# Kernel tuning notes

Measured on AMD Instinct MI355X. Metric: run time of the kernel, lower is better.

The kernel has to match this reference:

```python
import jax, jax.numpy as jnp
import numpy as np

DIM = 256   # state dimension
T = 8192    # number of time steps
B = 32      # batch of initial conditions
DT = 0.01   # time-grid spacing


def make_A(dim):
    # Faithful to MagnusLadder.__init__: diag=-0.1, superdiag=+0.5, subdiag=-0.5
    A = np.zeros((dim, dim), dtype=np.float32)
    np.fill_diagonal(A, -0.1)
    idx = np.arange(dim - 1)
    A[idx, idx + 1] = 0.5
    A[idx + 1, idx] = -0.5
    return jnp.asarray(A)


def setup_inputs() -> dict:
    key = jax.random.key(0)
    x0 = jax.random.normal(key, (DIM, B), dtype=jnp.float32)
    t = jnp.arange(T, dtype=jnp.float32) * DT  # uniform time grid, dt = DT
    A = make_A(DIM)
    return {"t": t, "x0": x0, "A": A}


def reference(t, x0, A):
    dt = t[1] - t[0]
    expAdt = jax.scipy.linalg.expm(A * dt)  # [dim, dim]

    def step(x, _):
        x = expAdt @ x  # [dim, B]
        return x, x

    _, traj = jax.lax.scan(step, x0, None, length=T - 1)  # [T-1, dim, B]
    return jnp.concatenate([x0[None], traj], axis=0)       # [T, dim, B]
```

## Files before the change

kernel.cpp:

```cpp
#include <hip/hip_runtime.h>
#include <hip/hip_bf16.h>


#define DIMN 256
#define BB   32
#define TSTEPS 8192
#define KT   32
#define DTF  0.01f

typedef __attribute__((ext_vector_type(8))) short bf16x8;
typedef __attribute__((ext_vector_type(4))) float f32x4;

static __device__ __forceinline__ short f2bf(float f) {
    union { __hip_bfloat16 h; short s; } u;
    u.h = __float2bfloat16(f);
    return u.s;
}

__global__ __launch_bounds__(256) void k1_prep(const float* __restrict__ x0,
                                               unsigned short* __restrict__ vfold,
                                               float* __restrict__ yr,
                                               float* __restrict__ yi) {
    const float PI257 = (float)(3.14159265358979323846 / 257.0);
    const float S257  = sqrtf(2.0f / 257.0f);
    const int g = blockIdx.x;
    const int t = threadIdx.x;

    __shared__ float x0s[256 * 32];
    __shared__ float ve[256], vo[256];

    if (g < 256) {
        const int j = g, J = j >> 1, p = j & 1, m = t;
        const int n = ((j + 1) * (m + 1)) % 514;
        const float v = S257 * sinf((float)n * PI257);
        float sgn;
        if (p == 0) sgn = (J & 1) ? -1.f : 1.f;
        else        sgn = (J & 1) ?  1.f : -1.f;
        vfold[p * 32768 + J * 256 + m] = (unsigned short)f2bf(sgn * v);
    } else {
        const int m = g - 256;
        for (int idx = t; idx < 256 * 32; idx += 256) x0s[idx] = x0[idx];
        const int n = ((m + 1) * (t + 1)) % 514;
        const float v = S257 * sinf((float)n * PI257);
        const int j = t;
        float veJ = 0.f, voJ = 0.f;
        if ((j & 1) == 0) veJ = ((j & 3) == 0) ? v : -v;
        else              voJ = ((j & 3) == 3) ? v : -v;
        ve[j] = veJ; vo[j] = voJ;
        __syncthreads();
        if (t < 32) {
            float sr = 0.f, si = 0.f;
            for (int jj = 0; jj < 256; ++jj) {
                sr += ve[jj] * x0s[jj * 32 + t];
                si += vo[jj] * x0s[jj * 32 + t];
            }
            yr[m * 32 + t] = sr;
            yi[m * 32 + t] = si;
        }
    }
}

__global__ __launch_bounds__(1024, 4) void k2_main(const unsigned short* __restrict__ vfold,
                                                   const float* __restrict__ yr,
                                                   const float* __restrict__ yi,
                                                   float* __restrict__ out) {
    __shared__ unsigned short ubuf[2][2][32 * 256];
    const float PI257 = (float)(3.14159265358979323846 / 257.0);
    const int tid  = threadIdx.x;
    const int lane = tid & 63;
    const int wave = tid >> 6;
    const int k0   = blockIdx.x * KT;

    const int b    = tid & 31;
    const int mblk = tid >> 5;
    const int m0   = mblk * 8;

    float c[8], s[8], cr[8], sr[8], yrv[8], yiv[8];
#pragma unroll
    for (int i = 0; i < 8; ++i) {
        const int m = m0 + i;
        const float lam = cosf((float)(m + 1) * PI257);
        const float th  = DTF * lam;
        const float a0  = (float)k0 * th;
        c[i]  = cosf(a0);  s[i]  = sinf(a0);
        cr[i] = cosf(th);  sr[i] = sinf(th);
        yrv[i] = yr[m * 32 + b];
        yiv[i] = yi[m * 32 + b];
    }

    const int p  = wave & 1;
    const int Tt = wave >> 1;
    const int rA = lane & 15;
    const int gA = lane >> 4;
    bf16x8 afr[8];
    {
        const unsigned short* arow = vfold + p * 32768 + (Tt * 16 + rA) * 256 + gA * 8;
#pragma unroll
        for (int ks = 0; ks < 8; ++ks)
            afr[ks] = *reinterpret_cast<const bf16x8*>(arow + ks * 32);
    }

    const int wOff = b * 256 + ((((m0 >> 5)) ^ (b & 7)) << 3) + (((m0 >> 3) & 3) << 6);

    float dec = __expf(-0.1f * DTF * (float)k0) * 1.0f;
    dec = expf(-0.1f * DTF * (float)k0);
    const float decr = expf(-0.1f * DTF);

    for (int kk = 0; kk < KT; ++kk) {
        const int dbi = kk & 1;
        bf16x8 vur, vui;
#pragma unroll
        for (int i = 0; i < 8; ++i) {
            const float urf = c[i] * yrv[i] - s[i] * yiv[i];
            const float uif = c[i] * yiv[i] + s[i] * yrv[i];
            vur[i] = f2bf(urf);
            vui[i] = f2bf(uif);
        }
        *reinterpret_cast<bf16x8*>(&ubuf[dbi][0][wOff]) = vur;
        *reinterpret_cast<bf16x8*>(&ubuf[dbi][1][wOff]) = vui;
#pragma unroll
        for (int i = 0; i < 8; ++i) {
            const float nc = c[i] * cr[i] - s[i] * sr[i];
            const float ns = s[i] * cr[i] + c[i] * sr[i];
            c[i] = nc; s[i] = ns;
        }
        __syncthreads();

        const unsigned short* uplane = &ubuf[dbi][p][0];
        float* outk = out + (size_t)(k0 + kk) * 8192;
#pragma unroll
        for (int nt = 0; nt < 2; ++nt) {
            const int brd = nt * 16 + (lane & 15);
            const int rbase = brd * 256 + (gA << 6);
            const int h = brd & 7;
            f32x4 acc = {0.f, 0.f, 0.f, 0.f};
#pragma unroll
            for (int ks = 0; ks < 8; ++ks) {
                const bf16x8 bfr =
                    *reinterpret_cast<const bf16x8*>(uplane + rbase + ((ks ^ h) << 3));
                acc = __builtin_amdgcn_mfma_f32_16x16x32_bf16(afr[ks], bfr, acc, 0, 0, 0);
            }
#pragma unroll
            for (int q = 0; q < 4; ++q) {
                const int j = 32 * Tt + 2 * (gA * 4 + q) + p;
                outk[j * 32 + brd] = acc[q] * dec;
            }
        }
        dec *= decr;
    }
}

extern "C" void kernel_launch(void* const* d_in, const int* in_sizes, int n_in,
                              void* d_out, int out_size, void* d_ws, size_t ws_size,
                              hipStream_t stream) {
    const float* x0 = (const float*)d_in[1];
    float* out = (float*)d_out;

    unsigned short* vfold = (unsigned short*)d_ws;
    float* yr = (float*)((char*)d_ws + 131072);
    float* yi = (float*)((char*)d_ws + 131072 + 32768);

    k1_prep<<<512, 256, 0, stream>>>(x0, vfold, yr, yi);
    k2_main<<<256, 1024, 0, stream>>>(vfold, yr, yi, out);
}
```

Baseline: 309.3 us.

## Halve block size, reuse B fragments across four row tiles, batch two steps per sync

k2_main now runs 512 threads per block. Each wave keeps four A row-tile fragments in registers and reuses every LDS B fragment across four MFMAs. Two time steps are produced per __syncthreads, and the rotation phase is computed directly with hardware sin/cos on a fractional-revolution angle instead of a recurrence. k1_prep spreads the projection reduction across all threads. The intent is fewer barriers and less LDS traffic per MFMA, at the cost of higher register pressure, larger shared memory, and possible precision change from the hardware trig.

```diff
diff --git a/kernel.cpp b/kernel.cpp
--- a/kernel.cpp
+++ b/kernel.cpp
@@ -28,6 +28,7 @@
 
     __shared__ float x0s[256 * 32];
     __shared__ float ve[256], vo[256];
+    __shared__ float psr[8][32], psi[8][32];
 
     if (g < 256) {
         const int j = g, J = j >> 1, p = j & 1, m = t;
@@ -48,105 +49,126 @@
         else              voJ = ((j & 3) == 3) ? v : -v;
         ve[j] = veJ; vo[j] = voJ;
         __syncthreads();
+        const int b = t & 31, jg = t >> 5;
+        float sr = 0.f, si = 0.f;
+#pragma unroll
+        for (int jj2 = 0; jj2 < 32; ++jj2) {
+            const int jj = jg * 32 + jj2;
+            sr += ve[jj] * x0s[jj * 32 + b];
+            si += vo[jj] * x0s[jj * 32 + b];
+        }
+        psr[jg][b] = sr; psi[jg][b] = si;
+        __syncthreads();
         if (t < 32) {
-            float sr = 0.f, si = 0.f;
-            for (int jj = 0; jj < 256; ++jj) {
-                sr += ve[jj] * x0s[jj * 32 + t];
-                si += vo[jj] * x0s[jj * 32 + t];
-            }
-            yr[m * 32 + t] = sr;
-            yi[m * 32 + t] = si;
+            float asr = 0.f, asi = 0.f;
+#pragma unroll
+            for (int q = 0; q < 8; ++q) { asr += psr[q][t]; asi += psi[q][t]; }
+            yr[m * 32 + t] = asr;
+            yi[m * 32 + t] = asi;
         }
     }
 }
 
-__global__ __launch_bounds__(1024, 4) void k2_main(const unsigned short* __restrict__ vfold,
-                                                   const float* __restrict__ yr,
-                                                   const float* __restrict__ yi,
-                                                   float* __restrict__ out) {
-    __shared__ unsigned short ubuf[2][2][32 * 256];
-    const float PI257 = (float)(3.14159265358979323846 / 257.0);
+__global__ __launch_bounds__(512, 2) void k2_main(const unsigned short* __restrict__ vfold,
+                                                  const float* __restrict__ yr,
+                                                  const float* __restrict__ yi,
+                                                  float* __restrict__ out) {
+    __shared__ unsigned short ubuf[2][2][2][8192];
+    const float PI257   = (float)(3.14159265358979323846 / 257.0);
+    const float INV2PI  = (float)(1.0 / (2.0 * 3.14159265358979323846));
     const int tid  = threadIdx.x;
     const int lane = tid & 63;
     const int wave = tid >> 6;
     const int k0   = blockIdx.x * KT;
 
-    const int b    = tid & 31;
-    const int mblk = tid >> 5;
-    const int m0   = mblk * 8;
+    const int bA   = tid & 15;
+    const int mblk = tid >> 4;
+    const int m0   = mblk << 3;
 
-    float c[8], s[8], cr[8], sr[8], yrv[8], yiv[8];
+    float threv[8], yrv0[8], yiv0[8], yrv1[8], yiv1[8];
 #pragma unroll
     for (int i = 0; i < 8; ++i) {
         const int m = m0 + i;
         const float lam = cosf((float)(m + 1) * PI257);
-        const float th  = DTF * lam;
-        const float a0  = (float)k0 * th;
-        c[i]  = cosf(a0);  s[i]  = sinf(a0);
-        cr[i] = cosf(th);  sr[i] = sinf(th);
-        yrv[i] = yr[m * 32 + b];
-        yiv[i] = yi[m * 32 + b];
+        threv[i] = DTF * lam * INV2PI;
+        yrv0[i] = yr[m * 32 + bA];       yiv0[i] = yi[m * 32 + bA];
+        yrv1[i] = yr[m * 32 + bA + 16];  yiv1[i] = yi[m * 32 + bA + 16];
     }
+    const int ksA = m0 >> 5, gA2 = (m0 >> 3) & 3;
+    const int wOff0 = bA * 256        + (((ksA ^ (bA & 7)))        << 3) + (gA2 << 6);
+    const int wOff1 = (bA + 16) * 256 + (((ksA ^ ((bA + 16) & 7))) << 3) + (gA2 << 6);
 
     const int p  = wave & 1;
-    const int Tt = wave >> 1;
+    const int nt = (wave >> 1) & 1;
+    const int rh = wave >> 2;
     const int rA = lane & 15;
     const int gA = lane >> 4;
-    bf16x8 afr[8];
-    {
-        const unsigned short* arow = vfold + p * 32768 + (Tt * 16 + rA) * 256 + gA * 8;
+    bf16x8 afr[4][8];
+#pragma unroll
+    for (int rt = 0; rt < 4; ++rt) {
+        const unsigned short* arow =
+            vfold + p * 32768 + (rh * 64 + rt * 16 + rA) * 256 + gA * 8;
 #pragma unroll
         for (int ks = 0; ks < 8; ++ks)
-            afr[ks] = *reinterpret_cast<const bf16x8*>(arow + ks * 32);
+            afr[rt][ks] = *reinterpret_cast<const bf16x8*>(arow + ks * 32);
     }
+    const int brd   = nt * 16 + rA;
+    const int h     = brd & 7;
+    const int rbase = brd * 256 + (gA << 6);
 
-    const int wOff = b * 256 + ((((m0 >> 5)) ^ (b & 7)) << 3) + (((m0 >> 3) & 3) << 6);
+    float dec = expf(-0.001f * (float)k0);
+    const float decr = expf(-0.001f);
 
-    float dec = __expf(-0.1f * DTF * (float)k0) * 1.0f;
-    dec = expf(-0.1f * DTF * (float)k0);
-    const float decr = expf(-0.1f * DTF);
-
-    for (int kk = 0; kk < KT; ++kk) {
-        const int dbi = kk & 1;
-        bf16x8 vur, vui;
+    for (int r = 0; r < KT / 2; ++r) {
+        const int d = r & 1;
 #pragma unroll
-        for (int i = 0; i < 8; ++i) {
-            const float urf = c[i] * yrv[i] - s[i] * yiv[i];
-            const float uif = c[i] * yiv[i] + s[i] * yrv[i];
-            vur[i] = f2bf(urf);
-            vui[i] = f2bf(uif);
-        }
-        *reinterpret_cast<bf16x8*>(&ubuf[dbi][0][wOff]) = vur;
-        *reinterpret_cast<bf16x8*>(&ubuf[dbi][1][wOff]) = vui;
+        for (int kw = 0; kw < 2; ++kw) {
+            const float kf = (float)(k0 + 2 * r + kw);
+            bf16x8 vur0, vui0, vur1, vui1;
 #pragma unroll
-        for (int i = 0; i < 8; ++i) {
-            const float nc = c[i] * cr[i] - s[i] * sr[i];
-            const float ns = s[i] * cr[i] + c[i] * sr[i];
-            c[i] = nc; s[i] = ns;
+            for (int i = 0; i < 8; ++i) {
+                const float ang = kf * threv[i];
+                const float fr  = ang - floorf(ang);
+                const float c   = __builtin_amdgcn_cosf(fr);
+                const float s   = __builtin_amdgcn_sinf(fr);
+                vur0[i] = f2bf(c * yrv0[i] - s * yiv0[i]);
+                vui0[i] = f2bf(c * yiv0[i] + s * yrv0[i]);
+                vur1[i] = f2bf(c * yrv1[i] - s * yiv1[i]);
+                vui1[i] = f2bf(c * yiv1[i] + s * yrv1[i]);
+            }
+            *reinterpret_cast<bf16x8*>(&ubuf[d][kw][0][wOff0]) = vur0;
+            *reinterpret_cast<bf16x8*>(&ubuf[d][kw][1][wOff0]) = vui0;
+            *reinterpret_cast<bf16x8*>(&ubuf[d][kw][0][wOff1]) = vur1;
+            *reinterpret_cast<bf16x8*>(&ubuf[d][kw][1][wOff1]) = vui1;
         }
         __syncthreads();
 
-        const unsigned short* uplane = &ubuf[dbi][p][0];
-        float* outk = out + (size_t)(k0 + kk) * 8192;
 #pragma unroll
-        for (int nt = 0; nt < 2; ++nt) {
-            const int brd = nt * 16 + (lane & 15);
-            const int rbase = brd * 256 + (gA << 6);
-            const int h = brd & 7;
-            f32x4 acc = {0.f, 0.f, 0.f, 0.f};
+        for (int kw = 0; kw < 2; ++kw) {
+            const unsigned short* up = &ubuf[d][kw][p][0];
+            float* outk = out + (size_t)(k0 + 2 * r + kw) * 8192;
+            f32x4 acc[4];
+#pragma unroll
+            for (int rt = 0; rt < 4; ++rt) acc[rt] = (f32x4){0.f, 0.f, 0.f, 0.f};
 #pragma unroll
             for (int ks = 0; ks < 8; ++ks) {
                 const bf16x8 bfr =
-                    *reinterpret_cast<const bf16x8*>(uplane + rbase + ((ks ^ h) << 3));
-                acc = __builtin_amdgcn_mfma_f32_16x16x32_bf16(afr[ks], bfr, acc, 0, 0, 0);
+                    *reinterpret_cast<const bf16x8*>(up + rbase + ((ks ^ h) << 3));
+#pragma unroll
+                for (int rt = 0; rt < 4; ++rt)
+                    acc[rt] = __builtin_amdgcn_mfma_f32_16x16x32_bf16(
+                        afr[rt][ks], bfr, acc[rt], 0, 0, 0);
             }
 #pragma unroll
-            for (int q = 0; q < 4; ++q) {
-                const int j = 32 * Tt + 2 * (gA * 4 + q) + p;
-                outk[j * 32 + brd] = acc[q] * dec;
+            for (int rt = 0; rt < 4; ++rt) {
+#pragma unroll
+                for (int q = 0; q < 4; ++q) {
+                    const int j = 2 * (rh * 64 + rt * 16 + gA * 4 + q) + p;
+                    outk[j * 32 + brd] = acc[rt][q] * dec;
+                }
             }
+            dec *= decr;
         }
-        dec *= decr;
     }
 }
 
@@ -161,5 +183,5 @@
     float* yi = (float*)((char*)d_ws + 131072 + 32768);
 
     k1_prep<<<512, 256, 0, stream>>>(x0, vfold, yr, yi);
-    k2_main<<<256, 1024, 0, stream>>>(vfold, yr, yi, out);
+    k2_main<<<256, 512, 0, stream>>>(vfold, yr, yi, out);
 }
```

Measured after the change: 272.8 us. 1.13x faster.
